# Kernel optimization log

Hardware: AMD Instinct MI355X
Metric: run time of the kernel (lower is better)

Reference implementation:

```python
import jax, jax.numpy as jnp
import numpy as np


def setup_inputs() -> dict:
    key = jax.random.key(0)
    k1, k2 = jax.random.split(key)
    B, L, D = 16, 4096, 1024
    X = jax.random.normal(k1, (B, L, D), dtype=jnp.float32)
    G = jax.random.normal(k2, (D, 2), dtype=jnp.float32) * (1.0 / np.sqrt(D))
    Gb = jnp.zeros((2,), dtype=jnp.float32)
    return {"X": X, "G": G, "Gb": Gb}


def reference(X, G, Gb):
    # X: (B, L, D) with L = 2*maxseg. For even i in [0, L-3]:
    #   out_p = X[:,i] * g0 + X[:,i+2] * g1, gates g = softmax(X[:,i+1] @ G + Gb)
    L = X.shape[1]
    lefts = X[:, 0:L - 2:2, :]   # (B, P, D), P = L/2 - 1
    mids = X[:, 1:L - 1:2, :]    # (B, P, D)
    rights = X[:, 2:L:2, :]      # (B, P, D)
    gates = jax.nn.softmax(jnp.einsum('bpd,dg->bpg', mids, G) + Gb, axis=-1)  # (B, P, 2)
    out = lefts * gates[..., 0:1] + rights * gates[..., 1:2]  # (B, P, D)
    return out
```

## Files before the change

### kernel.cpp

```cpp
#include <hip/hip_runtime.h>
#include <hip/hip_bf16.h>

constexpr int B = 16;
constexpr int L = 4096;
constexpr int D = 1024;
constexpr int P = (L - 2) / 2;

__global__ __launch_bounds__(256) void gated_cnn_kernel(
    const float* __restrict__ X,
    const float* __restrict__ G,
    const float* __restrict__ Gb,
    float* __restrict__ out) {
  const int idx = blockIdx.x;
  const int b = idx / P;
  const int p = idx - b * P;

  const float* xb    = X + (size_t)b * L * D;
  const float* left  = xb + (size_t)(2 * p + 0) * D;
  const float* mid   = xb + (size_t)(2 * p + 1) * D;
  const float* right = xb + (size_t)(2 * p + 2) * D;
  float* o = out + (size_t)idx * D;

  const int t = threadIdx.x;

  const float4 m  = ((const float4*)mid)[t];
  const float4 lf = ((const float4*)left)[t];
  const float4 rt = ((const float4*)right)[t];
  const float4 gA = ((const float4*)G)[2 * t];
  const float4 gB = ((const float4*)G)[2 * t + 1];

  float s0 = m.x * gA.x + m.y * gA.z + m.z * gB.x + m.w * gB.z;
  float s1 = m.x * gA.y + m.y * gA.w + m.z * gB.y + m.w * gB.w;

  #pragma unroll
  for (int off = 32; off > 0; off >>= 1) {
    s0 += __shfl_down(s0, off, 64);
    s1 += __shfl_down(s1, off, 64);
  }

  __shared__ float red[8];
  const int wave = t >> 6;
  if ((t & 63) == 0) {
    red[wave * 2 + 0] = s0;
    red[wave * 2 + 1] = s1;
  }
  __syncthreads();

  float t0 = red[0] + red[2] + red[4] + red[6] + Gb[0];
  float t1 = red[1] + red[3] + red[5] + red[7] + Gb[1];
  const float mx = fmaxf(t0, t1);
  const float e0 = __expf(t0 - mx);
  const float e1 = __expf(t1 - mx);
  const float inv = 1.0f / (e0 + e1);
  const float g0 = e0 * inv;
  const float g1 = e1 * inv;

  float4 r;
  r.x = lf.x * g0 + rt.x * g1;
  r.y = lf.y * g0 + rt.y * g1;
  r.z = lf.z * g0 + rt.z * g1;
  r.w = lf.w * g0 + rt.w * g1;
  ((float4*)o)[t] = r;
}

extern "C" void kernel_launch(void* const* d_in, const int* in_sizes, int n_in,
                              void* d_out, int out_size, void* d_ws, size_t ws_size,
                              hipStream_t stream) {
  const float* X  = (const float*)d_in[0];
  const float* G  = (const float*)d_in[1];
  const float* Gb = (const float*)d_in[2];
  float* out = (float*)d_out;

  gated_cnn_kernel<<<dim3(B * P), dim3(256), 0, stream>>>(X, G, Gb, out);
}
```

Baseline: 383.4 us.

## Process chunks of pairs per wave with row reuse and register prefetch

Each wavefront now handles eight consecutive output pairs of a batch instead of one block per pair. The gate weights stay in registers, the right row is reused as the next left row, and the next mid/right rows are prefetched while the current pair is computed. The cross-wave shared-memory reduction and barrier are replaced by a wave-level xor shuffle reduction. This cuts redundant global loads and per-block overhead, but leaves fewer, longer-lived waves with higher register pressure.

```diff
diff --git a/kernel.cpp b/kernel.cpp
--- a/kernel.cpp
+++ b/kernel.cpp
@@ -1,66 +1,98 @@
 #include <hip/hip_runtime.h>
-#include <hip/hip_bf16.h>
 
 constexpr int B = 16;
 constexpr int L = 4096;
 constexpr int D = 1024;
 constexpr int P = (L - 2) / 2;
+constexpr int RQ = D / 4;
+
+constexpr int C   = 8;
+constexpr int CPB = (P + C - 1) / C;
+constexpr int WPB = 4;
+constexpr int NBLOCKS = (B * CPB) / WPB;
 
 __global__ __launch_bounds__(256) void gated_cnn_kernel(
     const float* __restrict__ X,
     const float* __restrict__ G,
     const float* __restrict__ Gb,
     float* __restrict__ out) {
-  const int idx = blockIdx.x;
-  const int b = idx / P;
-  const int p = idx - b * P;
+  const int lane = threadIdx.x & 63;
+  const int gw   = blockIdx.x * WPB + (threadIdx.x >> 6);
+  const int b    = gw / CPB;
+  const int c    = gw - b * CPB;
+  const int p0   = c * C;
+  const int np   = min(C, P - p0);
 
-  const float* xb    = X + (size_t)b * L * D;
-  const float* left  = xb + (size_t)(2 * p + 0) * D;
-  const float* mid   = xb + (size_t)(2 * p + 1) * D;
-  const float* right = xb + (size_t)(2 * p + 2) * D;
-  float* o = out + (size_t)idx * D;
+  const float4* Gf4 = (const float4*)G;
+  float4 gA[4], gB[4];
+#pragma unroll
+  for (int j = 0; j < 4; ++j) {
+    gA[j] = Gf4[2 * lane + 128 * j];
+    gB[j] = Gf4[2 * lane + 128 * j + 1];
+  }
+  const float gb0 = Gb[0];
+  const float gb1 = Gb[1];
 
-  const int t = threadIdx.x;
+  const float4* xb = (const float4*)(X + (size_t)b * L * D);
+  const float4* row = xb + (size_t)(2 * p0) * RQ + lane;
+  float4* ob = (float4*)(out + ((size_t)b * P + p0) * (size_t)D);
 
-  const float4 m  = ((const float4*)mid)[t];
-  const float4 lf = ((const float4*)left)[t];
-  const float4 rt = ((const float4*)right)[t];
-  const float4 gA = ((const float4*)G)[2 * t];
-  const float4 gB = ((const float4*)G)[2 * t + 1];
+  float4 lf[4], m[4], r[4];
+#pragma unroll
+  for (int j = 0; j < 4; ++j) lf[j] = row[64 * j];
+  row += RQ;
+#pragma unroll
+  for (int j = 0; j < 4; ++j) m[j] = row[64 * j];
+  row += RQ;
+#pragma unroll
+  for (int j = 0; j < 4; ++j) r[j] = row[64 * j];
 
-  float s0 = m.x * gA.x + m.y * gA.z + m.z * gB.x + m.w * gB.z;
-  float s1 = m.x * gA.y + m.y * gA.w + m.z * gB.y + m.w * gB.w;
+  for (int i = 0; i < np; ++i) {
+    const bool more = (i + 1 < np);
+    const float4* mrow = row + (more ? RQ : 0);
+    const float4* rrow = row + (more ? 2 * RQ : 0);
+    float4 mn[4], rn[4];
+#pragma unroll
+    for (int j = 0; j < 4; ++j) mn[j] = mrow[64 * j];
+#pragma unroll
+    for (int j = 0; j < 4; ++j) rn[j] = rrow[64 * j];
 
-  #pragma unroll
-  for (int off = 32; off > 0; off >>= 1) {
-    s0 += __shfl_down(s0, off, 64);
-    s1 += __shfl_down(s1, off, 64);
+    float s0 = 0.f, s1 = 0.f;
+#pragma unroll
+    for (int j = 0; j < 4; ++j) {
+      s0 += m[j].x * gA[j].x + m[j].y * gA[j].z + m[j].z * gB[j].x + m[j].w * gB[j].z;
+      s1 += m[j].x * gA[j].y + m[j].y * gA[j].w + m[j].z * gB[j].y + m[j].w * gB[j].w;
+    }
+#pragma unroll
+    for (int off = 1; off < 64; off <<= 1) {
+      s0 += __shfl_xor(s0, off, 64);
+      s1 += __shfl_xor(s1, off, 64);
+    }
+
+    const float t0 = s0 + gb0;
+    const float t1 = s1 + gb1;
+    const float mx = fmaxf(t0, t1);
+    const float e0 = __expf(t0 - mx);
+    const float e1 = __expf(t1 - mx);
+    const float inv = 1.0f / (e0 + e1);
+    const float g0 = e0 * inv;
+    const float g1 = e1 * inv;
+
+    float4* o = ob + (size_t)i * RQ + lane;
+#pragma unroll
+    for (int j = 0; j < 4; ++j) {
+      float4 v;
+      v.x = lf[j].x * g0 + r[j].x * g1;
+      v.y = lf[j].y * g0 + r[j].y * g1;
+      v.z = lf[j].z * g0 + r[j].z * g1;
+      v.w = lf[j].w * g0 + r[j].w * g1;
+      o[64 * j] = v;
+    }
+
+#pragma unroll
+    for (int j = 0; j < 4; ++j) { lf[j] = r[j]; m[j] = mn[j]; r[j] = rn[j]; }
+    row += 2 * RQ;
   }
-
-  __shared__ float red[8];
-  const int wave = t >> 6;
-  if ((t & 63) == 0) {
-    red[wave * 2 + 0] = s0;
-    red[wave * 2 + 1] = s1;
-  }
-  __syncthreads();
-
-  float t0 = red[0] + red[2] + red[4] + red[6] + Gb[0];
-  float t1 = red[1] + red[3] + red[5] + red[7] + Gb[1];
-  const float mx = fmaxf(t0, t1);
-  const float e0 = __expf(t0 - mx);
-  const float e1 = __expf(t1 - mx);
-  const float inv = 1.0f / (e0 + e1);
-  const float g0 = e0 * inv;
-  const float g1 = e1 * inv;
-
-  float4 r;
-  r.x = lf.x * g0 + rt.x * g1;
-  r.y = lf.y * g0 + rt.y * g1;
-  r.z = lf.z * g0 + rt.z * g1;
-  r.w = lf.w * g0 + rt.w * g1;
-  ((float4*)o)[t] = r;
 }
 
 extern "C" void kernel_launch(void* const* d_in, const int* in_sizes, int n_in,
@@ -71,5 +103,5 @@
   const float* Gb = (const float*)d_in[2];
   float* out = (float*)d_out;
 
-  gated_cnn_kernel<<<dim3(B * P), dim3(256), 0, stream>>>(X, G, Gb, out);
+  gated_cnn_kernel<<<dim3(NBLOCKS), dim3(256), 0, stream>>>(X, G, Gb, out);
 }
```

Result: slower. 399.5 us (+4.2%).

## Process four pairs per block with shared row reuse and XCD-aware block swizzle

Applied to the files above, without the earlier changes.

Each workgroup now handles four consecutive output pairs by loading nine input rows once into registers, reusing the rows shared by adjacent pairs and amortizing the reduction and barrier cost. Blocks are remapped so contiguous chunks are grouped per XCD to improve L2 locality. This raises register use per thread and adds a tail path with clamped row indices.

```diff
diff --git a/kernel.cpp b/kernel.cpp
--- a/kernel.cpp
+++ b/kernel.cpp
@@ -1,66 +1,98 @@
 #include <hip/hip_runtime.h>
-#include <hip/hip_bf16.h>
 
 constexpr int B = 16;
 constexpr int L = 4096;
 constexpr int D = 1024;
 constexpr int P = (L - 2) / 2;
+constexpr int RQ = D / 4;
+constexpr int GP = 4;
+constexpr int CPB = (P + GP - 1) / GP;
+constexpr int NB = B * CPB;
+constexpr int NXCD = 8;
+constexpr int SPAN = NB / NXCD;
 
 __global__ __launch_bounds__(256) void gated_cnn_kernel(
     const float* __restrict__ X,
     const float* __restrict__ G,
     const float* __restrict__ Gb,
     float* __restrict__ out) {
-  const int idx = blockIdx.x;
-  const int b = idx / P;
-  const int p = idx - b * P;
-
-  const float* xb    = X + (size_t)b * L * D;
-  const float* left  = xb + (size_t)(2 * p + 0) * D;
-  const float* mid   = xb + (size_t)(2 * p + 1) * D;
-  const float* right = xb + (size_t)(2 * p + 2) * D;
-  float* o = out + (size_t)idx * D;
+  const int bid = blockIdx.x;
+  const int wg  = (bid % NXCD) * SPAN + bid / NXCD;
+  const int b   = wg / CPB;
+  const int c   = wg - b * CPB;
+  const int p0  = c * GP;
+  const int np  = min(GP, P - p0);
 
   const int t = threadIdx.x;
+  const float4* xb = (const float4*)(X + (size_t)b * L * D);
 
-  const float4 m  = ((const float4*)mid)[t];
-  const float4 lf = ((const float4*)left)[t];
-  const float4 rt = ((const float4*)right)[t];
+  float4 xr[9];
+  if (np == GP) {
+#pragma unroll
+    for (int r = 0; r < 9; ++r)
+      xr[r] = xb[(size_t)(2 * p0 + r) * RQ + t];
+  } else {
+#pragma unroll
+    for (int r = 0; r < 9; ++r) {
+      const int rr = min(2 * p0 + r, L - 1);
+      xr[r] = xb[(size_t)rr * RQ + t];
+    }
+  }
+
   const float4 gA = ((const float4*)G)[2 * t];
   const float4 gB = ((const float4*)G)[2 * t + 1];
+  const float gb0 = Gb[0];
+  const float gb1 = Gb[1];
 
-  float s0 = m.x * gA.x + m.y * gA.z + m.z * gB.x + m.w * gB.z;
-  float s1 = m.x * gA.y + m.y * gA.w + m.z * gB.y + m.w * gB.w;
-
-  #pragma unroll
-  for (int off = 32; off > 0; off >>= 1) {
-    s0 += __shfl_down(s0, off, 64);
-    s1 += __shfl_down(s1, off, 64);
+  float s[8];
+#pragma unroll
+  for (int i = 0; i < 4; ++i) {
+    const float4 m = xr[2 * i + 1];
+    s[2 * i + 0] = m.x * gA.x + m.y * gA.z + m.z * gB.x + m.w * gB.z;
+    s[2 * i + 1] = m.x * gA.y + m.y * gA.w + m.z * gB.y + m.w * gB.w;
   }
 
-  __shared__ float red[8];
+#pragma unroll
+  for (int off = 1; off < 64; off <<= 1) {
+#pragma unroll
+    for (int k = 0; k < 8; ++k) s[k] += __shfl_xor(s[k], off, 64);
+  }
+
+  __shared__ float red[4][8];
   const int wave = t >> 6;
   if ((t & 63) == 0) {
-    red[wave * 2 + 0] = s0;
-    red[wave * 2 + 1] = s1;
+#pragma unroll
+    for (int k = 0; k < 8; ++k) red[wave][k] = s[k];
   }
   __syncthreads();
 
-  float t0 = red[0] + red[2] + red[4] + red[6] + Gb[0];
-  float t1 = red[1] + red[3] + red[5] + red[7] + Gb[1];
-  const float mx = fmaxf(t0, t1);
-  const float e0 = __expf(t0 - mx);
-  const float e1 = __expf(t1 - mx);
-  const float inv = 1.0f / (e0 + e1);
-  const float g0 = e0 * inv;
-  const float g1 = e1 * inv;
+  float g0[4], g1[4];
+#pragma unroll
+  for (int i = 0; i < 4; ++i) {
+    const float t0 = red[0][2 * i] + red[1][2 * i] + red[2][2 * i] + red[3][2 * i] + gb0;
+    const float t1 = red[0][2 * i + 1] + red[1][2 * i + 1] + red[2][2 * i + 1] + red[3][2 * i + 1] + gb1;
+    const float mx = fmaxf(t0, t1);
+    const float e0 = __expf(t0 - mx);
+    const float e1 = __expf(t1 - mx);
+    const float inv = 1.0f / (e0 + e1);
+    g0[i] = e0 * inv;
+    g1[i] = e1 * inv;
+  }
 
-  float4 r;
-  r.x = lf.x * g0 + rt.x * g1;
-  r.y = lf.y * g0 + rt.y * g1;
-  r.z = lf.z * g0 + rt.z * g1;
-  r.w = lf.w * g0 + rt.w * g1;
-  ((float4*)o)[t] = r;
+  float4* ob = (float4*)(out + ((size_t)b * P + p0) * (size_t)D);
+#pragma unroll
+  for (int i = 0; i < 4; ++i) {
+    if (i < np) {
+      const float4 lf = xr[2 * i];
+      const float4 rt = xr[2 * i + 2];
+      float4 v;
+      v.x = lf.x * g0[i] + rt.x * g1[i];
+      v.y = lf.y * g0[i] + rt.y * g1[i];
+      v.z = lf.z * g0[i] + rt.z * g1[i];
+      v.w = lf.w * g0[i] + rt.w * g1[i];
+      ob[(size_t)i * RQ + t] = v;
+    }
+  }
 }
 
 extern "C" void kernel_launch(void* const* d_in, const int* in_sizes, int n_in,
@@ -71,5 +103,5 @@
   const float* Gb = (const float*)d_in[2];
   float* out = (float*)d_out;
 
-  gated_cnn_kernel<<<dim3(B * P), dim3(256), 0, stream>>>(X, G, Gb, out);
+  gated_cnn_kernel<<<dim3(NB), dim3(256), 0, stream>>>(X, G, Gb, out);
 }
```

Measured after the change: 390.0 us. Within noise of the previous version (+1.7%).
